# Performance work log

Hardware: AMD Instinct MI355X
Metric: run time of the kernel (lower is better)

The kernel has to match this reference:

```python
import jax, jax.numpy as jnp
import numpy as np

NUM_REGIONS = 3
REGION_SIZE = 384
IMG_SIZE = 512
PEAK_WINDOW = 5


def setup_inputs() -> dict:
    key = jax.random.key(0)
    ks = jax.random.split(key, 6)
    B, C, Hf, Wf = 32, 1024, 32, 32
    features = jax.random.normal(ks[0], (B, C, Hf, Wf), jnp.float32)
    cam_32x32 = jax.random.uniform(ks[1], (B, 32, 32), jnp.float32)
    original = jax.random.normal(ks[2], (B, 3, IMG_SIZE, IMG_SIZE), jnp.float32)
    def init_w(k, o, i):
        return jax.random.normal(k, (o, i), jnp.float32) * (1.0 / np.sqrt(i).astype(np.float32))
    w1 = init_w(ks[3], 512, C); b1 = jnp.zeros((512,), jnp.float32)
    w2 = init_w(ks[4], 256, 512); b2 = jnp.zeros((256,), jnp.float32)
    w3 = init_w(ks[5], 1, 256); b3 = jnp.zeros((1,), jnp.float32)
    return dict(features=features, cam_32x32=cam_32x32, original=original,
                w1=w1, b1=b1, w2=w2, b2=b2, w3=w3, b3=b3)


def _attention(features, w1, b1, w2, b2, w3, b3):
    # stack of 1x1 convs == per-pixel matmuls
    h = jax.nn.relu(jnp.einsum('bchw,oc->bohw', features, w1) + b1[None, :, None, None])
    h = jax.nn.relu(jnp.einsum('bchw,oc->bohw', h, w2) + b2[None, :, None, None])
    return jax.nn.sigmoid(jnp.einsum('bchw,oc->bohw', h, w3) + b3[None, :, None, None])


def _pick_peaks(score_map, K):
    # iterative argmax + square-window suppression (NMS-style peak picking)
    Hf, Wf = score_map.shape
    ys = jnp.arange(Hf)[:, None]
    xs = jnp.arange(Wf)[None, :]
    def step(scores, _):
        flat = jnp.argmax(scores)
        val = scores.reshape(-1)[flat]
        fy = (flat // Wf).astype(jnp.int32)
        fx = (flat % Wf).astype(jnp.int32)
        valid = val > 0.0
        fy = jnp.where(valid, fy, Hf // 2).astype(jnp.int32)
        fx = jnp.where(valid, fx, Wf // 2).astype(jnp.int32)
        supp = (jnp.abs(ys - fy) <= PEAK_WINDOW) & (jnp.abs(xs - fx) <= PEAK_WINDOW)
        return jnp.where(supp, jnp.zeros_like(scores), scores), jnp.stack([fy, fx])
    _, peaks = jax.lax.scan(step, score_map, None, length=K)
    return peaks  # [K, 2] (fy, fx)


def reference(features, cam_32x32, original, w1, b1, w2, b2, w3, b3):
    B, C, Hf, Wf = features.shape
    att = _attention(features, w1, b1, w2, b2, w3, b3)  # [B,1,Hf,Wf]
    # bilinear (align_corners=False) resize of CAM to feature grid
    cam_f = jax.image.resize(cam_32x32[:, None], (B, 1, Hf, Wf), 'bilinear')
    att = (att + cam_f) * 0.5

    peaks = jax.vmap(lambda m: _pick_peaks(m, NUM_REGIONS))(att[:, 0])  # [B,K,2]
    sy = IMG_SIZE / float(Hf)
    sx = IMG_SIZE / float(Wf)
    cy = jnp.floor(peaks[..., 0].astype(jnp.float32) * sy).astype(jnp.int32)
    cx = jnp.floor(peaks[..., 1].astype(jnp.float32) * sx).astype(jnp.int32)
    half = REGION_SIZE // 2
    # clamp-and-adjust logic collapses to a clip when img >= region size
    y1 = jnp.clip(cy - half, 0, IMG_SIZE - REGION_SIZE)
    x1 = jnp.clip(cx - half, 0, IMG_SIZE - REGION_SIZE)

    Cimg = original.shape[1]
    def crop_img(img, y1s, x1s):
        return jax.vmap(lambda y, x: jax.lax.dynamic_slice(
            img, (0, y, x), (Cimg, REGION_SIZE, REGION_SIZE)))(y1s, x1s)
    regions = jax.vmap(crop_img)(original, y1, x1)  # [B,K,3,rs,rs]
    regions = regions.reshape(B * NUM_REGIONS, Cimg, REGION_SIZE, REGION_SIZE)
    coords = jnp.stack([x1, y1, x1 + REGION_SIZE, y1 + REGION_SIZE], axis=-1)  # [B,K,4]
    return regions, coords, att
```

## Files before the change

### kernel.cpp

```cpp
#include <hip/hip_runtime.h>
#include <cstdint>
#include <cmath>


typedef float f4 __attribute__((ext_vector_type(4)));
typedef _Float16 f16x8 __attribute__((ext_vector_type(8)));
typedef int i4 __attribute__((ext_vector_type(4)));
typedef unsigned short u16x4 __attribute__((ext_vector_type(4)));

#define M_PIX 32768
#define COORDS_OFF 42467328
#define ATT_OFF 42467712
#define H1LO_OFF 8388608
#define H2_OFF 16777216
#define W1HI_OFF 25165824
#define W1LO_OFF 25427968
#define W2HI_OFF 25690112
#define W2LO_OFF 25755648

#define FH_T 8192
#define FL_T 10240

#define GLOAD16(gp, lp) \
    __builtin_amdgcn_global_load_lds( \
        (const __attribute__((address_space(1))) unsigned int*)(gp), \
        (__attribute__((address_space(3))) unsigned int*)(lp), 16, 0, 0)

__device__ __forceinline__ int swz(int row, int k16) {
    return ((row << 4) + (k16 >> 1)) ^ ((row & 7) << 2);
}

__device__ __forceinline__ int split_pack(float v0, float v1, int& lop) {
    _Float16 h0 = (_Float16)v0, h1 = (_Float16)v1;
    float r0 = v0 - (float)h0, r1 = v1 - (float)h1;
    _Float16 l0 = (_Float16)r0, l1 = (_Float16)r1;
    unsigned int uh0 = __builtin_bit_cast(unsigned short, h0);
    unsigned int uh1 = __builtin_bit_cast(unsigned short, h1);
    unsigned int ul0 = __builtin_bit_cast(unsigned short, l0);
    unsigned int ul1 = __builtin_bit_cast(unsigned short, l1);
    lop = (int)(ul0 | (ul1 << 16));
    return (int)(uh0 | (uh1 << 16));
}

__global__ __launch_bounds__(256) void split_plane(
    const float* __restrict__ src, unsigned short* __restrict__ hi,
    unsigned short* __restrict__ lo, int n4)
{
    const int i = blockIdx.x * 256 + threadIdx.x;
    if (i >= n4) return;
    f4 v = *(const f4*)(src + 4 * (size_t)i);
    u16x4 hv, lv;
    #pragma unroll
    for (int j = 0; j < 4; ++j) {
        _Float16 h = (_Float16)v[j];
        _Float16 l = (_Float16)(v[j] - (float)h);
        hv[j] = __builtin_bit_cast(unsigned short, h);
        lv[j] = __builtin_bit_cast(unsigned short, l);
    }
    *(u16x4*)(hi + 4 * (size_t)i) = hv;
    *(u16x4*)(lo + 4 * (size_t)i) = lv;
}

template<int MODE, int NBL>
__global__ __launch_bounds__(256, 2) void gemm_mfma(
    const unsigned short* __restrict__ WH, const unsigned short* __restrict__ WL,
    const void* __restrict__ FA, const void* __restrict__ FB,
    const float* __restrict__ bias, void* __restrict__ OA, void* __restrict__ OB,
    int Kdim, long fstride, int use_feat)
{
    __shared__ i4 ldsv[3072];
    int* lds = (int*)ldsv;

    const int t = threadIdx.x;
    const int lane = t & 63;
    const int wave = t >> 6;
    const int wn = wave >> 1, wp = wave & 1;

    const int f = blockIdx.x;
    const int nb = (f >> 3) & ((1 << NBL) - 1);
    const int pb = (f & 7) | ((f >> (3 + NBL)) << 3);
    const int n0  = nb * 128;
    const int px0 = pb * 128;

    const int rl = t & 127;
    const int kb = (t >> 7) * 16;

    const float* F32 = (const float*)FA;
    const unsigned short* FH16 = (const unsigned short*)FA;
    const unsigned short* FL16 = (const unsigned short*)FB;
    if constexpr (MODE == 0) {
        if (use_feat) F32 += ((size_t)(px0 >> 10) << 20) + (px0 & 1023) + rl;
        else          F32 += px0 + rl;
    } else {
        FH16 += px0 + rl;
        FL16 += px0 + rl;
    }

    int wg_off[2];
    #pragma unroll
    for (int j = 0; j < 2; ++j) {
        const int i  = 2 * wave + j;
        const int rL = 16 * i + (lane >> 2);
        const int r  = (rL & 4) ? (rL ^ 1) : rL;
        const int c  = (4 * (lane & 3)) ^ ((r & 3) << 2);
        wg_off[j] = (n0 + r) * Kdim + 2 * c;
    }

    f4 acc[4][4];
    #pragma unroll
    for (int i = 0; i < 4; ++i)
        #pragma unroll
        for (int j = 0; j < 4; ++j) acc[i][j] = (f4){0.f, 0.f, 0.f, 0.f};

    float fv[16];
    unsigned short hv[16], lv[16];

    auto W_GLOADS = [&](int buf, int k0) {
        const int wb = buf * 4096;
        #pragma unroll
        for (int j = 0; j < 2; ++j) {
            const int i = 2 * wave + j;
            GLOAD16(WH + wg_off[j] + k0, &lds[wb + 256 * i]);
            GLOAD16(WL + wg_off[j] + k0, &lds[wb + 2048 + 256 * i]);
        }
    };

    auto LOADS_F = [&](int k0) {
        if constexpr (MODE == 0) {
            #pragma unroll
            for (int j = 0; j < 16; ++j)
                fv[j] = F32[(size_t)(k0 + kb + j) * fstride];
        } else {
            #pragma unroll
            for (int j = 0; j < 16; ++j) {
                hv[j] = FH16[(size_t)(k0 + kb + j) * fstride];
                lv[j] = FL16[(size_t)(k0 + kb + j) * fstride];
            }
        }
    };

    auto STAGE_F = [&]() {
        #pragma unroll
        for (int g = 0; g < 2; ++g) {
            i4 hp, lp;
            if constexpr (MODE == 0) {
                #pragma unroll
                for (int j = 0; j < 4; ++j) {
                    int lo;
                    hp[j] = split_pack(fv[8 * g + 2 * j], fv[8 * g + 2 * j + 1], lo);
                    lp[j] = lo;
                }
            } else {
                #pragma unroll
                for (int j = 0; j < 4; ++j) {
                    hp[j] = (int)((unsigned int)hv[8 * g + 2 * j] |
                                  ((unsigned int)hv[8 * g + 2 * j + 1] << 16));
                    lp[j] = (int)((unsigned int)lv[8 * g + 2 * j] |
                                  ((unsigned int)lv[8 * g + 2 * j + 1] << 16));
                }
            }
            *(i4*)&lds[FH_T + swz(rl, kb + 8 * g)] = hp;
            *(i4*)&lds[FL_T + swz(rl, kb + 8 * g)] = lp;
        }
    };

    const int rA0 = 64 * wn + (lane & 15);
    const int rB0 = 64 * wp + (lane & 15);
    const int kg  = (lane >> 4) * 8;

    W_GLOADS(0, 0);
    LOADS_F(0);
    int cur = 0;
    for (int k0 = 0; k0 < Kdim; k0 += 32) {
        STAGE_F();
        __syncthreads();

        if (k0 + 32 < Kdim) { W_GLOADS(cur ^ 1, k0 + 32); LOADS_F(k0 + 32); }

        const int wb = cur * 4096;
        f16x8 bh[4], bl[4];
        #pragma unroll
        for (int nf = 0; nf < 4; ++nf) {
            bh[nf] = *(const f16x8*)&lds[FH_T + swz(rB0 + 16 * nf, kg)];
            bl[nf] = *(const f16x8*)&lds[FL_T + swz(rB0 + 16 * nf, kg)];
        }
        #pragma unroll
        for (int m = 0; m < 4; ++m) {
            f16x8 ah = *(const f16x8*)&lds[wb + swz(rA0 + 16 * m, kg)];
            f16x8 al = *(const f16x8*)&lds[wb + 2048 + swz(rA0 + 16 * m, kg)];
            #pragma unroll
            for (int nf = 0; nf < 4; ++nf) {
                acc[m][nf] = __builtin_amdgcn_mfma_f32_16x16x32_f16(ah, bh[nf], acc[m][nf], 0, 0, 0);
                acc[m][nf] = __builtin_amdgcn_mfma_f32_16x16x32_f16(ah, bl[nf], acc[m][nf], 0, 0, 0);
                acc[m][nf] = __builtin_amdgcn_mfma_f32_16x16x32_f16(al, bh[nf], acc[m][nf], 0, 0, 0);
            }
        }
        __syncthreads();
        cur ^= 1;
    }

    const int pxE = px0 + 64 * wp + (lane & 15);
    const int nE  = n0 + 64 * wn + 4 * (lane >> 4);
    unsigned short* o16a = (unsigned short*)OA;
    unsigned short* o16b = (unsigned short*)OB;
    float* o32 = (float*)OA;
    #pragma unroll
    for (int m = 0; m < 4; ++m) {
        const int n_m = nE + 16 * m;
        const f4 bv = *(const f4*)&bias[n_m];
        #pragma unroll
        for (int nf = 0; nf < 4; ++nf) {
            const int p = pxE + 16 * nf;
            #pragma unroll
            for (int r = 0; r < 4; ++r) {
                float v = fmaxf(acc[m][nf][r] + bv[r], 0.0f);
                if constexpr (MODE == 0) {
                    _Float16 h = (_Float16)v;
                    _Float16 l = (_Float16)(v - (float)h);
                    o16a[(size_t)(n_m + r) * M_PIX + p] = __builtin_bit_cast(unsigned short, h);
                    o16b[(size_t)(n_m + r) * M_PIX + p] = __builtin_bit_cast(unsigned short, l);
                } else {
                    o32[(size_t)(n_m + r) * M_PIX + p] = v;
                }
            }
        }
    }
}

__global__ __launch_bounds__(256) void layer3_att(
    const float* __restrict__ h2, const float* __restrict__ w3,
    const float* __restrict__ b3, const float* __restrict__ cam,
    float* __restrict__ att)
{
    const int p = blockIdx.x * 256 + threadIdx.x;
    float s = b3[0];
    #pragma unroll 8
    for (int k = 0; k < 256; ++k)
        s = fmaf(w3[k], h2[(size_t)k * M_PIX + p], s);
    const float sg = 1.0f / (1.0f + expf(-s));
    att[p] = (sg + cam[p]) * 0.5f;
}

__global__ __launch_bounds__(64) void peaks_kernel(
    const float* __restrict__ att, float* __restrict__ coords,
    int* __restrict__ wsyx)
{
    const int b = blockIdx.x;
    const int lane = threadIdx.x;
    __shared__ float s[1024];
    for (int i = lane; i < 1024; i += 64) s[i] = att[b * 1024 + i];
    __syncthreads();

    for (int kpk = 0; kpk < 3; ++kpk) {
        float bv = -1.0f;
        int bi = 0x7fffffff;
        for (int i = lane; i < 1024; i += 64) {
            float v = s[i];
            if (v > bv) { bv = v; bi = i; }
        }
        for (int off = 32; off >= 1; off >>= 1) {
            float ov = __shfl_down(bv, off);
            int   oi = __shfl_down(bi, off);
            if (ov > bv || (ov == bv && oi < bi)) { bv = ov; bi = oi; }
        }
        bv = __shfl(bv, 0);
        bi = __shfl(bi, 0);

        int fy, fx;
        if (bv > 0.0f) { fy = bi >> 5; fx = bi & 31; }
        else           { fy = 16;      fx = 16; }

        for (int i = lane; i < 1024; i += 64) {
            const int y = i >> 5, x = i & 31;
            const int dy = y > fy ? y - fy : fy - y;
            const int dx = x > fx ? x - fx : fx - x;
            if (dy <= 5 && dx <= 5) s[i] = 0.0f;
        }
        __syncthreads();

        if (lane == 0) {
            int y1 = fy * 16 - 192; y1 = y1 < 0 ? 0 : (y1 > 128 ? 128 : y1);
            int x1 = fx * 16 - 192; x1 = x1 < 0 ? 0 : (x1 > 128 ? 128 : x1);
            const int idx = b * 3 + kpk;
            coords[idx * 4 + 0] = (float)x1;
            coords[idx * 4 + 1] = (float)y1;
            coords[idx * 4 + 2] = (float)(x1 + 384);
            coords[idx * 4 + 3] = (float)(y1 + 384);
            wsyx[idx * 2 + 0] = y1;
            wsyx[idx * 2 + 1] = x1;
        }
        __syncthreads();
    }
}

__global__ __launch_bounds__(256) void crop_kernel(
    const float* __restrict__ orig, const int* __restrict__ wsyx,
    float* __restrict__ out)
{
    const int id = blockIdx.x * 256 + threadIdx.x;
    const int r    = id / (3 * 384 * 96);
    const int rem  = id - r * (3 * 384 * 96);
    const int c    = rem / (384 * 96);
    const int rem2 = rem - c * (384 * 96);
    const int row  = rem2 / 96;
    const int col  = (rem2 - row * 96) * 4;
    const int b = r / 3;
    const int y1 = wsyx[r * 2], x1 = wsyx[r * 2 + 1];
    const float* src = orig + (size_t)b * 786432 + (size_t)c * 262144
                     + (size_t)(y1 + row) * 512 + x1 + col;
    *(f4*)(out + (size_t)id * 4) = *(const f4*)src;
}

extern "C" void kernel_launch(void* const* d_in, const int* in_sizes, int n_in,
                              void* d_out, int out_size, void* d_ws, size_t ws_size,
                              hipStream_t stream)
{
    const float* features = (const float*)d_in[0];
    const float* cam      = (const float*)d_in[1];
    const float* original = (const float*)d_in[2];
    const float* w1 = (const float*)d_in[3];
    const float* b1 = (const float*)d_in[4];
    const float* w2 = (const float*)d_in[5];
    const float* b2 = (const float*)d_in[6];
    const float* w3 = (const float*)d_in[7];
    const float* b3 = (const float*)d_in[8];

    float* out    = (float*)d_out;
    unsigned short* h1hi = (unsigned short*)out;
    unsigned short* h1lo = (unsigned short*)(out + H1LO_OFF);
    float* h2     = out + H2_OFF;
    unsigned short* w1hi = (unsigned short*)(out + W1HI_OFF);
    unsigned short* w1lo = (unsigned short*)(out + W1LO_OFF);
    unsigned short* w2hi = (unsigned short*)(out + W2HI_OFF);
    unsigned short* w2lo = (unsigned short*)(out + W2LO_OFF);
    float* att    = out + ATT_OFF;
    float* coords = out + COORDS_OFF;
    int*   wsyx   = (int*)d_ws;

    dim3 b256(256);
    split_plane<<<dim3(512), b256, 0, stream>>>(w1, w1hi, w1lo, 131072);
    split_plane<<<dim3(128), b256, 0, stream>>>(w2, w2hi, w2lo, 32768);
    gemm_mfma<0, 2><<<dim3(1024), b256, 0, stream>>>(
        w1hi, w1lo, features, nullptr, b1, h1hi, h1lo, 1024, 1024L, 1);
    gemm_mfma<1, 1><<<dim3(512), b256, 0, stream>>>(
        w2hi, w2lo, h1hi, h1lo, b2, h2, nullptr, 512, (long)M_PIX, 0);
    layer3_att<<<dim3(128), b256, 0, stream>>>(h2, w3, b3, cam, att);
    peaks_kernel<<<dim3(32), dim3(64), 0, stream>>>(att, coords, wsyx);
    crop_kernel<<<dim3(41472), b256, 0, stream>>>(original, wsyx, out);
}
```

Measured before the change: 479.6 us.

## Pre-split features into tiled fp16 hi/lo layout and DMA both GEMM operands to LDS

Adds a split_tile_f kernel that converts the fp32 features into pre-swizzled, k-block-tiled fp16 hi/lo planes. The layer-1 GEMM, split into two halves over pixel blocks to bound scratch use, then loads both operands straight into LDS with global_load_lds instead of strided per-thread loads plus register staging. The layer-1 epilogue writes h1 in the same tiled hi/lo layout through LDS, so layer 2 also gets contiguous DMA loads, and the main loop drops one barrier per iteration. The cost is extra kernel launches and an extra global round-trip for the split feature tensor.

After: 513.1 us. 1.07x slower.

```diff
diff --git a/kernel.cpp b/kernel.cpp
--- a/kernel.cpp
+++ b/kernel.cpp
@@ -11,15 +11,16 @@
 #define M_PIX 32768
 #define COORDS_OFF 42467328
 #define ATT_OFF 42467712
-#define H1LO_OFF 8388608
-#define H2_OFF 16777216
-#define W1HI_OFF 25165824
-#define W1LO_OFF 25427968
-#define W2HI_OFF 25690112
-#define W2LO_OFF 25755648
-
-#define FH_T 8192
-#define FL_T 10240
+
+#define FHI_OFF 0
+#define FLO_OFF 8388608
+#define H2_OFF 0
+#define H1HI_OFF 16777216
+#define H1LO_OFF 25165824
+#define W1HI_OFF 33554432
+#define W1LO_OFF 33816576
+#define W2HI_OFF 34078720
+#define W2LO_OFF 34144256
 
 #define GLOAD16(gp, lp) \
     __builtin_amdgcn_global_load_lds( \
@@ -61,106 +62,96 @@
     *(u16x4*)(lo + 4 * (size_t)i) = lv;
 }
 
-template<int MODE, int NBL>
+__global__ __launch_bounds__(256) void split_tile_f(
+    const float* __restrict__ feat, unsigned int* __restrict__ fhi,
+    unsigned int* __restrict__ flo, int pb_base)
+{
+    const int blk = blockIdx.x;
+    const int lpb = blk >> 5, kb = blk & 31;
+    const int pb  = pb_base + lpb;
+    const int t = threadIdx.x;
+    __shared__ float ftile[32][128];
+
+    const int k   = t >> 3;
+    const int pxl = (t & 7) * 16;
+    const int px0 = pb * 128;
+    const size_t base = ((size_t)(px0 >> 10) << 20)
+                      + (size_t)(kb * 32 + k) * 1024 + (px0 & 1023) + pxl;
+    #pragma unroll
+    for (int j = 0; j < 4; ++j)
+        *(f4*)&ftile[k][pxl + 4 * j] = *(const f4*)(feat + base + 4 * j);
+    __syncthreads();
+
+    const int L   = 8 * t;
+    const int rL  = L >> 4;
+    const int row = rL ^ ((rL >> 2) & 1);
+    const int cb  = L & 15;
+    unsigned int hp[8], lp[8];
+    #pragma unroll
+    for (int j = 0; j < 8; ++j) {
+        const int kint = (cb + j) ^ ((row & 3) << 2);
+        int lo;
+        int hi = split_pack(ftile[2 * kint][row], ftile[2 * kint + 1][row], lo);
+        hp[j] = (unsigned int)hi; lp[j] = (unsigned int)lo;
+    }
+    unsigned int* oh = fhi + (((size_t)lpb * 32 + kb) << 11) + L;
+    unsigned int* ol = flo + (((size_t)lpb * 32 + kb) << 11) + L;
+    *(i4*)(oh)     = *(i4*)&hp[0];
+    *(i4*)(oh + 4) = *(i4*)&hp[4];
+    *(i4*)(ol)     = *(i4*)&lp[0];
+    *(i4*)(ol + 4) = *(i4*)&lp[4];
+}
+
+template<int MODE, int NBL, int NKB>
 __global__ __launch_bounds__(256, 2) void gemm_mfma(
     const unsigned short* __restrict__ WH, const unsigned short* __restrict__ WL,
-    const void* __restrict__ FA, const void* __restrict__ FB,
+    const unsigned int* __restrict__ FH, const unsigned int* __restrict__ FL,
     const float* __restrict__ bias, void* __restrict__ OA, void* __restrict__ OB,
-    int Kdim, long fstride, int use_feat)
-{
-    __shared__ i4 ldsv[3072];
-    int* lds = (int*)ldsv;
+    int pb_base)
+{
+    constexpr int Kdim = NKB * 32;
+    __shared__ int lds[16384];
 
     const int t = threadIdx.x;
     const int lane = t & 63;
     const int wave = t >> 6;
     const int wn = wave >> 1, wp = wave & 1;
 
-    const int f = blockIdx.x;
-    const int nb = (f >> 3) & ((1 << NBL) - 1);
-    const int pb = (f & 7) | ((f >> (3 + NBL)) << 3);
+    const int f   = blockIdx.x;
+    const int nb  = (f >> 3) & ((1 << NBL) - 1);
+    const int lpb = (f & 7) | ((f >> (3 + NBL)) << 3);
     const int n0  = nb * 128;
-    const int px0 = pb * 128;
-
-    const int rl = t & 127;
-    const int kb = (t >> 7) * 16;
-
-    const float* F32 = (const float*)FA;
-    const unsigned short* FH16 = (const unsigned short*)FA;
-    const unsigned short* FL16 = (const unsigned short*)FB;
-    if constexpr (MODE == 0) {
-        if (use_feat) F32 += ((size_t)(px0 >> 10) << 20) + (px0 & 1023) + rl;
-        else          F32 += px0 + rl;
-    } else {
-        FH16 += px0 + rl;
-        FL16 += px0 + rl;
-    }
+    const int px0 = (pb_base + lpb) * 128;
 
     int wg_off[2];
     #pragma unroll
     for (int j = 0; j < 2; ++j) {
         const int i  = 2 * wave + j;
         const int rL = 16 * i + (lane >> 2);
-        const int r  = (rL & 4) ? (rL ^ 1) : rL;
+        const int r  = rL ^ ((rL >> 2) & 1);
         const int c  = (4 * (lane & 3)) ^ ((r & 3) << 2);
         wg_off[j] = (n0 + r) * Kdim + 2 * c;
     }
 
+    const unsigned int* fhb = FH + ((size_t)lpb * NKB << 11) + 256 * (2 * wave) + 4 * lane;
+    const unsigned int* flb = FL + ((size_t)lpb * NKB << 11) + 256 * (2 * wave) + 4 * lane;
+
     f4 acc[4][4];
     #pragma unroll
     for (int i = 0; i < 4; ++i)
         #pragma unroll
         for (int j = 0; j < 4; ++j) acc[i][j] = (f4){0.f, 0.f, 0.f, 0.f};
 
-    float fv[16];
-    unsigned short hv[16], lv[16];
-
-    auto W_GLOADS = [&](int buf, int k0) {
-        const int wb = buf * 4096;
+    auto DMA = [&](int buf, int kb) {
+        const int wb = buf * 4096, fb = 8192 + buf * 4096;
+        const int k0 = kb * 32;
         #pragma unroll
         for (int j = 0; j < 2; ++j) {
             const int i = 2 * wave + j;
             GLOAD16(WH + wg_off[j] + k0, &lds[wb + 256 * i]);
             GLOAD16(WL + wg_off[j] + k0, &lds[wb + 2048 + 256 * i]);
-        }
-    };
-
-    auto LOADS_F = [&](int k0) {
-        if constexpr (MODE == 0) {
-            #pragma unroll
-            for (int j = 0; j < 16; ++j)
-                fv[j] = F32[(size_t)(k0 + kb + j) * fstride];
-        } else {
-            #pragma unroll
-            for (int j = 0; j < 16; ++j) {
-                hv[j] = FH16[(size_t)(k0 + kb + j) * fstride];
-                lv[j] = FL16[(size_t)(k0 + kb + j) * fstride];
-            }
-        }
-    };
-
-    auto STAGE_F = [&]() {
-        #pragma unroll
-        for (int g = 0; g < 2; ++g) {
-            i4 hp, lp;
-            if constexpr (MODE == 0) {
-                #pragma unroll
-                for (int j = 0; j < 4; ++j) {
-                    int lo;
-                    hp[j] = split_pack(fv[8 * g + 2 * j], fv[8 * g + 2 * j + 1], lo);
-                    lp[j] = lo;
-                }
-            } else {
-                #pragma unroll
-                for (int j = 0; j < 4; ++j) {
-                    hp[j] = (int)((unsigned int)hv[8 * g + 2 * j] |
-                                  ((unsigned int)hv[8 * g + 2 * j + 1] << 16));
-                    lp[j] = (int)((unsigned int)lv[8 * g + 2 * j] |
-                                  ((unsigned int)lv[8 * g + 2 * j + 1] << 16));
-                }
-            }
-            *(i4*)&lds[FH_T + swz(rl, kb + 8 * g)] = hp;
-            *(i4*)&lds[FL_T + swz(rl, kb + 8 * g)] = lp;
+            GLOAD16(fhb + ((size_t)kb << 11) + 256 * j, &lds[fb + 256 * i]);
+            GLOAD16(flb + ((size_t)kb << 11) + 256 * j, &lds[fb + 2048 + 256 * i]);
         }
     };
 
@@ -168,21 +159,18 @@
     const int rB0 = 64 * wp + (lane & 15);
     const int kg  = (lane >> 4) * 8;
 
-    W_GLOADS(0, 0);
-    LOADS_F(0);
+    DMA(0, 0);
     int cur = 0;
-    for (int k0 = 0; k0 < Kdim; k0 += 32) {
-        STAGE_F();
-        __syncthreads();
-
-        if (k0 + 32 < Kdim) { W_GLOADS(cur ^ 1, k0 + 32); LOADS_F(k0 + 32); }
-
-        const int wb = cur * 4096;
+    for (int kb = 0; kb < NKB; ++kb) {
+        __syncthreads();
+        if (kb + 1 < NKB) DMA(cur ^ 1, kb + 1);
+
+        const int wb = cur * 4096, fb = 8192 + cur * 4096;
         f16x8 bh[4], bl[4];
         #pragma unroll
         for (int nf = 0; nf < 4; ++nf) {
-            bh[nf] = *(const f16x8*)&lds[FH_T + swz(rB0 + 16 * nf, kg)];
-            bl[nf] = *(const f16x8*)&lds[FL_T + swz(rB0 + 16 * nf, kg)];
+            bh[nf] = *(const f16x8*)&lds[fb + swz(rB0 + 16 * nf, kg)];
+            bl[nf] = *(const f16x8*)&lds[fb + 2048 + swz(rB0 + 16 * nf, kg)];
         }
         #pragma unroll
         for (int m = 0; m < 4; ++m) {
@@ -195,33 +183,60 @@
                 acc[m][nf] = __builtin_amdgcn_mfma_f32_16x16x32_f16(al, bh[nf], acc[m][nf], 0, 0, 0);
             }
         }
-        __syncthreads();
         cur ^= 1;
     }
 
-    const int pxE = px0 + 64 * wp + (lane & 15);
-    const int nE  = n0 + 64 * wn + 4 * (lane >> 4);
-    unsigned short* o16a = (unsigned short*)OA;
-    unsigned short* o16b = (unsigned short*)OB;
-    float* o32 = (float*)OA;
-    #pragma unroll
-    for (int m = 0; m < 4; ++m) {
-        const int n_m = nE + 16 * m;
-        const f4 bv = *(const f4*)&bias[n_m];
-        #pragma unroll
-        for (int nf = 0; nf < 4; ++nf) {
-            const int p = pxE + 16 * nf;
+    if constexpr (MODE == 0) {
+        __syncthreads();
+        #pragma unroll
+        for (int m = 0; m < 4; ++m) {
+            const int n_l = 64 * wn + 4 * (lane >> 4) + 16 * m;
+            const f4 bv = *(const f4*)&bias[n0 + n_l];
+            const int kb_l = n_l >> 5;
             #pragma unroll
-            for (int r = 0; r < 4; ++r) {
-                float v = fmaxf(acc[m][nf][r] + bv[r], 0.0f);
-                if constexpr (MODE == 0) {
-                    _Float16 h = (_Float16)v;
-                    _Float16 l = (_Float16)(v - (float)h);
-                    o16a[(size_t)(n_m + r) * M_PIX + p] = __builtin_bit_cast(unsigned short, h);
-                    o16b[(size_t)(n_m + r) * M_PIX + p] = __builtin_bit_cast(unsigned short, l);
-                } else {
-                    o32[(size_t)(n_m + r) * M_PIX + p] = v;
-                }
+            for (int nf = 0; nf < 4; ++nf) {
+                const int row = 64 * wp + (lane & 15) + 16 * nf;
+                float v0 = fmaxf(acc[m][nf][0] + bv[0], 0.0f);
+                float v1 = fmaxf(acc[m][nf][1] + bv[1], 0.0f);
+                float v2 = fmaxf(acc[m][nf][2] + bv[2], 0.0f);
+                float v3 = fmaxf(acc[m][nf][3] + bv[3], 0.0f);
+                int lo0, lo1;
+                int hi0 = split_pack(v0, v1, lo0);
+                int hi1 = split_pack(v2, v3, lo1);
+                const int i0 = swz(row, (n_l & 31));
+                const int i1 = swz(row, (n_l & 31) + 2);
+                lds[kb_l * 2048 + i0]        = hi0;
+                lds[kb_l * 2048 + i1]        = hi1;
+                lds[8192 + kb_l * 2048 + i0] = lo0;
+                lds[8192 + kb_l * 2048 + i1] = lo1;
+            }
+        }
+        __syncthreads();
+        const int g = t >> 5;
+        const int l32 = t & 31;
+        const int pb = pb_base + lpb;
+        unsigned int* h1hi = (unsigned int*)OA;
+        unsigned int* h1lo = (unsigned int*)OB;
+        unsigned int* dst = ((g >> 2) ? h1lo : h1hi)
+                          + (((size_t)pb * 16 + 4 * nb + (g & 3)) << 11) + 64 * l32;
+        const int* src = &lds[(g >> 2) * 8192 + (g & 3) * 2048 + 64 * l32];
+        #pragma unroll
+        for (int q = 0; q < 16; ++q)
+            *(i4*)(dst + 4 * q) = *(const i4*)(src + 4 * q);
+    } else {
+        float* o32 = (float*)OA;
+        const int pxE = px0 + 64 * wp + (lane & 15);
+        const int nE  = n0 + 64 * wn + 4 * (lane >> 4);
+        #pragma unroll
+        for (int m = 0; m < 4; ++m) {
+            const int n_m = nE + 16 * m;
+            const f4 bv = *(const f4*)&bias[n_m];
+            #pragma unroll
+            for (int nf = 0; nf < 4; ++nf) {
+                const int p = pxE + 16 * nf;
+                #pragma unroll
+                for (int r = 0; r < 4; ++r)
+                    o32[(size_t)(n_m + r) * M_PIX + p] = fmaxf(acc[m][nf][r] + bv[r], 0.0f);
             }
         }
     }
@@ -325,10 +340,12 @@
     const float* w3 = (const float*)d_in[7];
     const float* b3 = (const float*)d_in[8];
 
-    float* out    = (float*)d_out;
-    unsigned short* h1hi = (unsigned short*)out;
-    unsigned short* h1lo = (unsigned short*)(out + H1LO_OFF);
-    float* h2     = out + H2_OFF;
+    float* out = (float*)d_out;
+    unsigned int* fhi  = (unsigned int*)(out + FHI_OFF);
+    unsigned int* flo  = (unsigned int*)(out + FLO_OFF);
+    unsigned int* h1hi = (unsigned int*)(out + H1HI_OFF);
+    unsigned int* h1lo = (unsigned int*)(out + H1LO_OFF);
+    float* h2 = out + H2_OFF;
     unsigned short* w1hi = (unsigned short*)(out + W1HI_OFF);
     unsigned short* w1lo = (unsigned short*)(out + W1LO_OFF);
     unsigned short* w2hi = (unsigned short*)(out + W2HI_OFF);
@@ -340,10 +357,14 @@
     dim3 b256(256);
     split_plane<<<dim3(512), b256, 0, stream>>>(w1, w1hi, w1lo, 131072);
     split_plane<<<dim3(128), b256, 0, stream>>>(w2, w2hi, w2lo, 32768);
-    gemm_mfma<0, 2><<<dim3(1024), b256, 0, stream>>>(
-        w1hi, w1lo, features, nullptr, b1, h1hi, h1lo, 1024, 1024L, 1);
-    gemm_mfma<1, 1><<<dim3(512), b256, 0, stream>>>(
-        w2hi, w2lo, h1hi, h1lo, b2, h2, nullptr, 512, (long)M_PIX, 0);
+    split_tile_f<<<dim3(4096), b256, 0, stream>>>(features, fhi, flo, 0);
+    gemm_mfma<0, 2, 32><<<dim3(512), b256, 0, stream>>>(
+        w1hi, w1lo, fhi, flo, b1, h1hi, h1lo, 0);
+    split_tile_f<<<dim3(4096), b256, 0, stream>>>(features, fhi, flo, 128);
+    gemm_mfma<0, 2, 32><<<dim3(512), b256, 0, stream>>>(
+        w1hi, w1lo, fhi, flo, b1, h1hi, h1lo, 128);
+    gemm_mfma<1, 1, 16><<<dim3(512), b256, 0, stream>>>(
+        w2hi, w2lo, h1hi, h1lo, b2, h2, nullptr, 0);
     layer3_att<<<dim3(128), b256, 0, stream>>>(h2, w3, b3, cam, att);
     peaks_kernel<<<dim3(32), dim3(64), 0, stream>>>(att, coords, wsyx);
     crop_kernel<<<dim3(41472), b256, 0, stream>>>(original, wsyx, out);
```
